# Kernel optimization log

Measured on AMD Instinct MI355X. Metric: run time of the kernel, lower is better.

The kernel has to match this reference:

```python
import jax, jax.numpy as jnp
import numpy as np

NUM_HEADS = 16
THETA = 10000.0


def _rope(x, cos, sin):
    # x: [B, H, S, d_k]; cos/sin: [S, d_k//2]
    x_even = x[..., 0::2]
    x_odd = x[..., 1::2]
    out_even = x_even * cos - x_odd * sin
    out_odd = x_odd * cos + x_even * sin
    # interleave back to original even/odd layout
    return jnp.stack([out_even, out_odd], axis=-1).reshape(x.shape)


def setup_inputs() -> dict:
    key = jax.random.key(0)
    ks = jax.random.split(key, 5)
    B, S, D = 2, 2048, 1024
    std = 2.0 / (D + D)
    return {
        "x": jax.random.normal(ks[0], (B, S, D), dtype=jnp.float32),
        "w_q": jax.random.normal(ks[1], (D, D), dtype=jnp.float32) * std,
        "w_k": jax.random.normal(ks[2], (D, D), dtype=jnp.float32) * std,
        "w_v": jax.random.normal(ks[3], (D, D), dtype=jnp.float32) * std,
        "w_o": jax.random.normal(ks[4], (D, D), dtype=jnp.float32) * std,
    }


def reference(x, w_q, w_k, w_v, w_o):
    B, S, D = x.shape
    H = NUM_HEADS
    d_k = D // H

    # QKV projections: x @ W.T
    q = jnp.einsum('bsd,ed->bse', x, w_q).reshape(B, S, H, d_k).transpose(0, 2, 1, 3)
    k = jnp.einsum('bsd,ed->bse', x, w_k).reshape(B, S, H, d_k).transpose(0, 2, 1, 3)
    v = jnp.einsum('bsd,ed->bse', x, w_v).reshape(B, S, H, d_k).transpose(0, 2, 1, 3)

    # RoPE (token_positions = arange(S))
    pos = jnp.arange(S, dtype=jnp.float32)
    inv_freq = 1.0 / (THETA ** (2.0 * jnp.arange(d_k // 2, dtype=jnp.float32) / d_k))
    angles = pos[:, None] * inv_freq[None, :]  # [S, d_k//2]
    cos, sin = jnp.cos(angles), jnp.sin(angles)
    q = _rope(q, cos, sin)
    k = _rope(k, cos, sin)

    # causal attention
    scores = jnp.einsum('bhqd,bhkd->bhqk', q, k) / jnp.sqrt(jnp.float32(d_k))
    causal = jnp.tril(jnp.ones((S, S), dtype=bool))
    scores = jnp.where(causal[None, None], scores, -jnp.inf)
    attn = jax.nn.softmax(scores, axis=-1)
    out = jnp.einsum('bhqk,bhkd->bhqd', attn, v)  # [B, H, S, d_k]

    out = out.transpose(0, 2, 1, 3).reshape(B, S, D)
    return jnp.einsum('bsd,ed->bse', out, w_o)
```

## Files before the change

### kernel.cpp

```cpp
#include <hip/hip_runtime.h>

typedef unsigned short u16;
typedef unsigned int u32;
typedef short bf16x8 __attribute__((ext_vector_type(8)));
typedef float f32x4 __attribute__((ext_vector_type(4)));

#define CSC 0.18033688011112042f

__device__ __forceinline__ u16 f2bf(float f) {
    union { float f; unsigned u; } x; x.f = f;
    unsigned r = x.u + 0x7fffu + ((x.u >> 16) & 1u);
    return (u16)(r >> 16);
}
__device__ __forceinline__ float bf2f(u16 v) {
    union { unsigned u; float f; } x; x.u = ((unsigned)v) << 16;
    return x.f;
}
__device__ __forceinline__ u32 cvt_pk_bf16(float lo, float hi) {
    u32 r;
    asm("v_cvt_pk_bf16_f32 %0, %1, %2" : "=v"(r) : "v"(lo), "v"(hi));
    return r;
}
__device__ __forceinline__ float exp2_fast(float x) {
#if __has_builtin(__builtin_amdgcn_exp2f)
    return __builtin_amdgcn_exp2f(x);
#else
    return exp2f(x);
#endif
}
__device__ __forceinline__ void gl_lds16(const u16* g, u16* l) {
#if __has_builtin(__builtin_amdgcn_global_load_lds)
    __builtin_amdgcn_global_load_lds(
        (const __attribute__((address_space(1))) unsigned int*)g,
        (__attribute__((address_space(3))) unsigned int*)l, 16, 0, 0);
#else
    *(bf16x8*)l = *(const bf16x8*)g;
#endif
}
__device__ __forceinline__ int ileave(int x) {
    return (x < 16) ? (x << 1) : (((x - 16) << 1) | 1);
}

__global__ void cvt_all_kernel(const float* __restrict__ x, const float* __restrict__ wq,
                               const float* __restrict__ wk, const float* __restrict__ wv,
                               const float* __restrict__ wo,
                               u16* __restrict__ xb, u16* __restrict__ qkvw,
                               u16* __restrict__ ow) {
    int i = blockIdx.x * 256 + threadIdx.x;
    const float4* src;
    ushort4* dst;
    if (i < 1048576) {
        src = (const float4*)x + i;
        dst = (ushort4*)xb + i;
    } else {
        int r = i - 1048576;
        int m = r >> 18;
        int off = r & 262143;
        const float* s4 = (m == 0) ? wq : (m == 1) ? wk : (m == 2) ? wv : wo;
        u16* d = (m < 3) ? (qkvw + (size_t)m * 1048576) : ow;
        src = (const float4*)s4 + off;
        dst = (ushort4*)d + off;
    }
    float4 v = *src;
    ushort4 o;
    o.x = f2bf(v.x); o.y = f2bf(v.y); o.z = f2bf(v.z); o.w = f2bf(v.w);
    *dst = o;
}

__global__ void rope_kernel(u16* __restrict__ qb, u16* __restrict__ kb) {
    int idx = blockIdx.x * 256 + threadIdx.x;
    u16* buf;
    float scale;
    if (blockIdx.y == 0) { buf = qb; scale = CSC; } else { buf = kb; scale = 1.0f; }
    int g   = idx & 7;
    int row = idx >> 3;
    int s   = row & 2047;
    u16* p = buf + (size_t)row * 64 + g * 8;
    bf16x8 v = *(bf16x8*)p;
    bf16x8 o;
    #pragma unroll
    for (int q = 0; q < 4; ++q) {
        int i = g * 4 + q;
        float inv = exp2_fast((float)i * -0.4152410118609203f);
        float ang = (float)s * inv;
        float sn, cs;
        sincosf(ang, &sn, &cs);
        float e  = bf2f(((u16*)&v)[2 * q]);
        float od = bf2f(((u16*)&v)[2 * q + 1]);
        ((u16*)&o)[2 * q]     = f2bf((e * cs - od * sn) * scale);
        ((u16*)&o)[2 * q + 1] = f2bf((od * cs + e * sn) * scale);
    }
    *(bf16x8*)p = o;
}

__global__ __launch_bounds__(256) void gemm_qkv(const u16* __restrict__ A,
                                                const u16* __restrict__ Bw,
                                                u16* __restrict__ C, int K) {
    __shared__ __align__(16) u16 SH[8448];
    u16* As = SH;
    u16* Bs = SH + 4096;
    const int tid  = threadIdx.x;
    const int bm   = blockIdx.x * 128;
    const int bn   = blockIdx.y * 128;
    const int wave = tid >> 6, lane = tid & 63;
    const int wm   = (wave >> 1) * 64, wn = (wave & 1) * 64;
    const int l16  = lane & 15, quad = lane >> 4;
    const int mat  = bn >> 10;

    f32x4 acc[4][4];
    #pragma unroll
    for (int i = 0; i < 4; i++)
        #pragma unroll
        for (int j = 0; j < 4; j++)
            #pragma unroll
            for (int e = 0; e < 4; e++) acc[i][j][e] = 0.0f;

    const int srow = tid >> 2, scol = (tid & 3) * 8;
    const u16* gA0 = A  + (size_t)(bm + srow) * K + scol;
    const u16* gA1 = A  + (size_t)(bm + 64 + srow) * K + scol;
    const u16* gB0 = Bw + (size_t)(bn + srow) * K + scol;
    const u16* gB1 = Bw + (size_t)(bn + 64 + srow) * K + scol;
    u16* lA0 = &As[(size_t)tid * 8];
    u16* lA1 = &As[(size_t)(tid + 256) * 8];
    u16* lB0 = &Bs[(size_t)tid * 8];
    u16* lB1 = &Bs[(size_t)(tid + 256) * 8];

    for (int k0 = 0; k0 < K; k0 += 32) {
        __syncthreads();
        gl_lds16(gA0 + k0, lA0);
        gl_lds16(gA1 + k0, lA1);
        gl_lds16(gB0 + k0, lB0);
        gl_lds16(gB1 + k0, lB1);
        __syncthreads();
        bf16x8 af[4], bfr[4];
        #pragma unroll
        for (int i = 0; i < 4; i++) af[i]  = *(const bf16x8*)&As[(wm + i * 16 + l16) * 32 + quad * 8];
        #pragma unroll
        for (int j = 0; j < 4; j++) bfr[j] = *(const bf16x8*)&Bs[(wn + j * 16 + l16) * 32 + quad * 8];
        #pragma unroll
        for (int i = 0; i < 4; i++)
            #pragma unroll
            for (int j = 0; j < 4; j++)
                acc[i][j] = __builtin_amdgcn_mfma_f32_16x16x32_bf16(af[i], bfr[j], acc[i][j], 0, 0, 0);
    }

    const int b  = bm >> 11, sb = bm & 2047;
    if (mat < 2) {
        #pragma unroll
        for (int pass = 0; pass < 2; ++pass) {
            __syncthreads();
            if ((wn >> 6) == pass) {
                #pragma unroll
                for (int i = 0; i < 4; i++)
                    #pragma unroll
                    for (int j = 0; j < 4; j++)
                        #pragma unroll
                        for (int r = 0; r < 4; r++) {
                            int rl = wm + i * 16 + quad * 4 + r;
                            int cl = j * 16 + l16;
                            SH[rl * 66 + cl] = f2bf(acc[i][j][r]);
                        }
            }
            __syncthreads();
            int rl   = tid >> 1;
            int half = (tid & 1) * 32;
            int c    = (bn + pass * 64) & 1023;
            int h    = c >> 6;
            int s    = sb + rl;
            u16* dst = C + (size_t)mat * 4194304 +
                       (((size_t)(b * 16 + h) * 2048 + s) * 64) + half;
            const u16* srcp = &SH[rl * 66 + half];
            #pragma unroll
            for (int kk = 0; kk < 4; ++kk)
                *(bf16x8*)(dst + kk * 8) = *(const bf16x8*)(srcp + kk * 8);
        }
    } else {
        #pragma unroll
        for (int pass = 0; pass < 2; ++pass) {
            __syncthreads();
            if ((wn >> 6) == pass) {
                #pragma unroll
                for (int i = 0; i < 4; i++)
                    #pragma unroll
                    for (int j = 0; j < 4; j++)
                        #pragma unroll
                        for (int r = 0; r < 4; r++) {
                            int row = j * 16 + l16;
                            int ml  = wm + i * 16 + quad * 4 + r;
                            int sp  = (ml & ~31) | ileave(ml & 31);
                            SH[row * 130 + sp] = f2bf(acc[i][j][r]);
                        }
            }
            __syncthreads();
            int row = tid >> 2, seg = tid & 3;
            int cc  = (bn + pass * 64 + row) & 1023;
            int h = cc >> 6, dv = cc & 63;
            u16* dst = C + (size_t)8388608 +
                       (((size_t)(b * 16 + h) * 64 + dv) * 2048) + sb + seg * 32;
            const u16* srcp = &SH[row * 130 + seg * 32];
            #pragma unroll
            for (int kk = 0; kk < 4; ++kk)
                *(bf16x8*)(dst + kk * 8) = *(const bf16x8*)(srcp + kk * 8);
        }
    }
}

__global__ __launch_bounds__(256, 2) void gemm_out(const u16* __restrict__ A,
                                                   const u16* __restrict__ Bw,
                                                   float* __restrict__ C, int K) {
    __shared__ __align__(16) u16 As[128 * 32];
    __shared__ __align__(16) u16 Bs[64 * 32];
    const int tid  = threadIdx.x;
    const int bm   = blockIdx.x * 128;
    const int bn   = blockIdx.y * 64;
    const int wave = tid >> 6, lane = tid & 63;
    const int wm   = wave * 32;
    const int l16  = lane & 15, quad = lane >> 4;

    f32x4 acc[2][4];
    #pragma unroll
    for (int i = 0; i < 2; i++)
        #pragma unroll
        for (int j = 0; j < 4; j++)
            #pragma unroll
            for (int e = 0; e < 4; e++) acc[i][j][e] = 0.0f;

    const int srow = tid >> 2, scol = (tid & 3) * 8;
    const u16* gA0 = A  + (size_t)(bm + srow) * K + scol;
    const u16* gA1 = A  + (size_t)(bm + 64 + srow) * K + scol;
    const u16* gB0 = Bw + (size_t)(bn + srow) * K + scol;
    u16* lA0 = &As[(size_t)tid * 8];
    u16* lA1 = &As[(size_t)(tid + 256) * 8];
    u16* lB0 = &Bs[(size_t)tid * 8];

    for (int k0 = 0; k0 < K; k0 += 32) {
        __syncthreads();
        gl_lds16(gA0 + k0, lA0);
        gl_lds16(gA1 + k0, lA1);
        gl_lds16(gB0 + k0, lB0);
        __syncthreads();
        bf16x8 af[2], bfr[4];
        #pragma unroll
        for (int i = 0; i < 2; i++) af[i]  = *(const bf16x8*)&As[(wm + i * 16 + l16) * 32 + quad * 8];
        #pragma unroll
        for (int j = 0; j < 4; j++) bfr[j] = *(const bf16x8*)&Bs[(j * 16 + l16) * 32 + quad * 8];
        #pragma unroll
        for (int i = 0; i < 2; i++)
            #pragma unroll
            for (int j = 0; j < 4; j++)
                acc[i][j] = __builtin_amdgcn_mfma_f32_16x16x32_bf16(af[i], bfr[j], acc[i][j], 0, 0, 0);
    }

    #pragma unroll
    for (int i = 0; i < 2; i++)
        #pragma unroll
        for (int j = 0; j < 4; j++)
            #pragma unroll
            for (int r = 0; r < 4; r++) {
                int mr = bm + wm + i * 16 + quad * 4 + r;
                int nc = bn + j * 16 + l16;
                C[(size_t)mr * 1024 + nc] = acc[i][j][r];
            }
}

__global__ __launch_bounds__(256, 2) void attn_kernel(const u16* __restrict__ Q,
                                                      const u16* __restrict__ Kb,
                                                      const u16* __restrict__ Vt,
                                                      u16* __restrict__ Oout) {
    __shared__ __align__(16) u16 KV[2][8192];
    __shared__ __align__(16) u16 PW[8 * 1024];
    const int tid  = threadIdx.x;
    const int wave = tid >> 6, lane = tid & 63;
    const int l16  = lane & 15, quad = lane >> 4;
    const int bid  = blockIdx.x;
    const int j    = (bid >> 3) & 15;
    const int bh   = (bid & 7) * 4 + (bid >> 7);
    const int T    = 32 - j;
    const int qA0  = j * 64 + wave * 16;
    const int qB0  = (31 - j) * 64 + wave * 16;

    const u16* Qh = Q  + (size_t)bh * 2048 * 64;
    const u16* Kh = Kb + (size_t)bh * 2048 * 64;
    const u16* Vh = Vt + (size_t)bh * 64 * 2048;

    bf16x8 qAf0 = *(const bf16x8*)&Qh[(size_t)(qA0 + l16) * 64 + quad * 8];
    bf16x8 qAf1 = *(const bf16x8*)&Qh[(size_t)(qA0 + l16) * 64 + 32 + quad * 8];
    bf16x8 qBf0 = *(const bf16x8*)&Qh[(size_t)(qB0 + l16) * 64 + quad * 8];
    bf16x8 qBf1 = *(const bf16x8*)&Qh[(size_t)(qB0 + l16) * 64 + 32 + quad * 8];

    f32x4 oA[4], oB[4];
    float lsA[4], lsB[4];
    #pragma unroll
    for (int t = 0; t < 4; t++)
        #pragma unroll
        for (int e = 0; e < 4; e++) { oA[t][e] = 0.0f; oB[t][e] = 0.0f; }
    #pragma unroll
    for (int r = 0; r < 4; r++) { lsA[r] = 0.0f; lsB[r] = 0.0f; }

    const int srow = tid >> 2;
    const int scs  = (((tid & 3) ^ ((tid >> 3) & 3))) * 8;
    const u16* gK = Kh + (size_t)srow * 64 + scs;
    const u16* gV = Vh + (size_t)srow * 2048 + scs;

    const int cswz = (quad ^ ((l16 >> 1) & 3)) * 8;
    const int psw0 = ((quad ^ (l16 & 7)) << 3);
    const int psw1 = (((quad ^ (l16 & 7)) ^ 4) << 3);

    u16* pw16B = PW + wave * 2048;
    u16* pw16A = pw16B + 1024;
    u32* pw32B = (u32*)pw16B;
    u32* pw32A = (u32*)pw16A;

    auto stage = [&](int t, int buf) {
        u16* base = KV[buf];
        gl_lds16(gK + (size_t)t * 4096,      base + (size_t)tid * 8);
        gl_lds16(gK + (size_t)t * 4096 + 32, base + 2048 + (size_t)tid * 8);
        gl_lds16(gV + (size_t)t * 64,        base + 4096 + (size_t)tid * 8);
        gl_lds16(gV + (size_t)t * 64 + 32,   base + 6144 + (size_t)tid * 8);
    };

    auto qk_pack = [&](const bf16x8& q0f, const bf16x8& q1f, bf16x8* kf0, bf16x8* kf1,
                       float* ls, u32* pw32, int q0, int kbase, bool diag) {
        f32x4 s[4];
        #pragma unroll
        for (int n = 0; n < 4; n++) {
            #pragma unroll
            for (int e = 0; e < 4; e++) s[n][e] = 0.0f;
            s[n] = __builtin_amdgcn_mfma_f32_16x16x32_bf16(q0f, kf0[n], s[n], 0, 0, 0);
            s[n] = __builtin_amdgcn_mfma_f32_16x16x32_bf16(q1f, kf1[n], s[n], 0, 0, 0);
        }
        float p[4][4];
        #pragma unroll
        for (int n = 0; n < 4; n++)
            #pragma unroll
            for (int r = 0; r < 4; r++) {
                float v = exp2_fast(s[n][r]);
                if (diag) {
                    int row = q0 + quad * 4 + r;
                    v = (kbase + n * 16 + l16 > row) ? 0.0f : v;
                }
                p[n][r] = v;
                ls[r] += v;
            }
        #pragma unroll
        for (int c = 0; c < 2; c++)
            #pragma unroll
            for (int r = 0; r < 4; r++) {
                int prow = quad * 4 + r;
                int pj   = (((c * 4 + (l16 >> 2)) ^ (prow & 7)) << 2) | (l16 & 3);
                pw32[prow * 32 + pj] = cvt_pk_bf16(p[2 * c][r], p[2 * c + 1][r]);
            }
    };

    auto pv = [&](u16* pw16, bf16x8* vf0, bf16x8* vf1, f32x4* o) {
        bf16x8 pf0 = *(const bf16x8*)&pw16[l16 * 64 + psw0];
        bf16x8 pf1 = *(const bf16x8*)&pw16[l16 * 64 + psw1];
        #pragma unroll
        for (int dn = 0; dn < 4; dn++) {
            o[dn] = __builtin_amdgcn_mfma_f32_16x16x32_bf16(pf0, vf0[dn], o[dn], 0, 0, 0);
            o[dn] = __builtin_amdgcn_mfma_f32_16x16x32_bf16(pf1, vf1[dn], o[dn], 0, 0, 0);
        }
    };

    stage(0, 0);
    for (int t = 0; t < T; ++t) {
        __syncthreads();
        if (t + 1 < T) stage(t + 1, (t + 1) & 1);
        const u16* B = KV[t & 1];
        bf16x8 kf0[4], kf1[4], vf0[4], vf1[4];
        #pragma unroll
        for (int n = 0; n < 4; n++) {
            int ri = (n * 16 + l16) * 32 + cswz;
            kf0[n] = *(const bf16x8*)&B[ri];
            kf1[n] = *(const bf16x8*)&B[2048 + ri];
            vf0[n] = *(const bf16x8*)&B[4096 + ri];
            vf1[n] = *(const bf16x8*)&B[6144 + ri];
        }
        const int kbase = t * 64;
        const bool hasA = (t <= j);

        qk_pack(qBf0, qBf1, kf0, kf1, lsB, pw32B, qB0, kbase, t == T - 1);
        if (hasA)
            qk_pack(qAf0, qAf1, kf0, kf1, lsA, pw32A, qA0, kbase, t == j);

        asm volatile("s_waitcnt lgkmcnt(0)" ::: "memory");

        pv(pw16B, vf0, vf1, oB);
        if (hasA)
            pv(pw16A, vf0, vf1, oA);
    }

    #pragma unroll
    for (int off = 1; off < 16; off <<= 1)
        #pragma unroll
        for (int r = 0; r < 4; r++) {
            lsA[r] += __shfl_xor(lsA[r], off);
            lsB[r] += __shfl_xor(lsB[r], off);
        }

    const int b = bh >> 4, h = bh & 15;
    #pragma unroll
    for (int r = 0; r < 4; r++) {
        float iA = 1.0f / lsA[r];
        float iB = 1.0f / lsB[r];
        int sA = qA0 + quad * 4 + r;
        int sB = qB0 + quad * 4 + r;
        #pragma unroll
        for (int dn = 0; dn < 4; dn++) {
            int d = h * 64 + dn * 16 + l16;
            Oout[((size_t)b * 2048 + sA) * 1024 + d] = f2bf(oA[dn][r] * iA);
            Oout[((size_t)b * 2048 + sB) * 1024 + d] = f2bf(oB[dn][r] * iB);
        }
    }
}

extern "C" void kernel_launch(void* const* d_in, const int* in_sizes, int n_in,
                              void* d_out, int out_size, void* d_ws, size_t ws_size,
                              hipStream_t stream) {
    const float* x  = (const float*)d_in[0];
    const float* wq = (const float*)d_in[1];
    const float* wk = (const float*)d_in[2];
    const float* wv = (const float*)d_in[3];
    const float* wo = (const float*)d_in[4];
    float* out = (float*)d_out;

    const int M = 4096, D = 1024;
    u16* xb    = (u16*)d_ws;
    u16* qkvw  = xb   + (size_t)M * D;
    u16* ow    = qkvw + (size_t)3 * D * D;
    u16* qkv   = ow   + (size_t)D * D;
    u16* qb    = qkv;
    u16* kb    = qkv + (size_t)M * D;
    u16* vtb   = qkv + (size_t)2 * M * D;
    u16* aob   = qkv + (size_t)3 * M * D;

    cvt_all_kernel<<<8192, 256, 0, stream>>>(x, wq, wk, wv, wo, xb, qkvw, ow);

    dim3 gq(32, 24);
    gemm_qkv<<<gq, 256, 0, stream>>>(xb, qkvw, qkv, D);

    dim3 gr(2048, 2);
    rope_kernel<<<gr, 256, 0, stream>>>(qb, kb);

    attn_kernel<<<512, 256, 0, stream>>>(qb, kb, vtb, aob);

    dim3 go(32, 16);
    gemm_out<<<go, 256, 0, stream>>>(aob, ow, out, D);
}
```

Measured before the change: 192.9 us.

## Double-buffer LDS tiles and XOR-swizzle columns in projection GEMMs

Both the QKV and output projection GEMMs now ping-pong between two LDS buffers. The next K-slice's global-to-LDS load is issued before the MFMA work on the current slice, which lets the loads overlap compute and removes one barrier per iteration. The 8-element column chunk is also XOR-swizzled by row bits on both the store and the fragment-read sides, to cut LDS bank conflicts on the 32-wide rows. The cost is double the LDS per block, which could lower occupancy, especially for gemm_out with its two-blocks-per-CU launch bound.

```diff
diff --git a/kernel.cpp b/kernel.cpp
--- a/kernel.cpp
+++ b/kernel.cpp
@@ -96,9 +96,8 @@
 __global__ __launch_bounds__(256) void gemm_qkv(const u16* __restrict__ A,
                                                 const u16* __restrict__ Bw,
                                                 u16* __restrict__ C, int K) {
-    __shared__ __align__(16) u16 SH[8448];
-    u16* As = SH;
-    u16* Bs = SH + 4096;
+    __shared__ __align__(16) u16 SB[16384];
+    u16* SH = SB;
     const int tid  = threadIdx.x;
     const int bm   = blockIdx.x * 128;
     const int bn   = blockIdx.y * 128;
@@ -115,33 +114,41 @@
             #pragma unroll
             for (int e = 0; e < 4; e++) acc[i][j][e] = 0.0f;
 
-    const int srow = tid >> 2, scol = (tid & 3) * 8;
+    const int srow = tid >> 2;
+    const int scol = (((tid & 3) ^ ((tid >> 3) & 3))) * 8;
     const u16* gA0 = A  + (size_t)(bm + srow) * K + scol;
     const u16* gA1 = A  + (size_t)(bm + 64 + srow) * K + scol;
     const u16* gB0 = Bw + (size_t)(bn + srow) * K + scol;
     const u16* gB1 = Bw + (size_t)(bn + 64 + srow) * K + scol;
-    u16* lA0 = &As[(size_t)tid * 8];
-    u16* lA1 = &As[(size_t)(tid + 256) * 8];
-    u16* lB0 = &Bs[(size_t)tid * 8];
-    u16* lB1 = &Bs[(size_t)(tid + 256) * 8];
-
+    const int csw = (quad ^ ((l16 >> 1) & 3)) * 8;
+
+    auto stage = [&](int k0, int buf) {
+        u16* As = SB + buf * 8192;
+        u16* Bs = As + 4096;
+        gl_lds16(gA0 + k0, As + (size_t)tid * 8);
+        gl_lds16(gA1 + k0, As + (size_t)(tid + 256) * 8);
+        gl_lds16(gB0 + k0, Bs + (size_t)tid * 8);
+        gl_lds16(gB1 + k0, Bs + (size_t)(tid + 256) * 8);
+    };
+
+    stage(0, 0);
+    int cur = 0;
     for (int k0 = 0; k0 < K; k0 += 32) {
         __syncthreads();
-        gl_lds16(gA0 + k0, lA0);
-        gl_lds16(gA1 + k0, lA1);
-        gl_lds16(gB0 + k0, lB0);
-        gl_lds16(gB1 + k0, lB1);
-        __syncthreads();
+        if (k0 + 32 < K) stage(k0 + 32, cur ^ 1);
+        const u16* As = SB + cur * 8192;
+        const u16* Bs = As + 4096;
         bf16x8 af[4], bfr[4];
         #pragma unroll
-        for (int i = 0; i < 4; i++) af[i]  = *(const bf16x8*)&As[(wm + i * 16 + l16) * 32 + quad * 8];
-        #pragma unroll
-        for (int j = 0; j < 4; j++) bfr[j] = *(const bf16x8*)&Bs[(wn + j * 16 + l16) * 32 + quad * 8];
+        for (int i = 0; i < 4; i++) af[i]  = *(const bf16x8*)&As[(wm + i * 16 + l16) * 32 + csw];
+        #pragma unroll
+        for (int j = 0; j < 4; j++) bfr[j] = *(const bf16x8*)&Bs[(wn + j * 16 + l16) * 32 + csw];
         #pragma unroll
         for (int i = 0; i < 4; i++)
             #pragma unroll
             for (int j = 0; j < 4; j++)
                 acc[i][j] = __builtin_amdgcn_mfma_f32_16x16x32_bf16(af[i], bfr[j], acc[i][j], 0, 0, 0);
+        cur ^= 1;
     }
 
     const int b  = bm >> 11, sb = bm & 2047;
@@ -208,8 +215,7 @@
 __global__ __launch_bounds__(256, 2) void gemm_out(const u16* __restrict__ A,
                                                    const u16* __restrict__ Bw,
                                                    float* __restrict__ C, int K) {
-    __shared__ __align__(16) u16 As[128 * 32];
-    __shared__ __align__(16) u16 Bs[64 * 32];
+    __shared__ __align__(16) u16 SB[12288];
     const int tid  = threadIdx.x;
     const int bm   = blockIdx.x * 128;
     const int bn   = blockIdx.y * 64;
@@ -225,30 +231,38 @@
             #pragma unroll
             for (int e = 0; e < 4; e++) acc[i][j][e] = 0.0f;
 
-    const int srow = tid >> 2, scol = (tid & 3) * 8;
+    const int srow = tid >> 2;
+    const int scol = (((tid & 3) ^ ((tid >> 3) & 3))) * 8;
     const u16* gA0 = A  + (size_t)(bm + srow) * K + scol;
     const u16* gA1 = A  + (size_t)(bm + 64 + srow) * K + scol;
     const u16* gB0 = Bw + (size_t)(bn + srow) * K + scol;
-    u16* lA0 = &As[(size_t)tid * 8];
-    u16* lA1 = &As[(size_t)(tid + 256) * 8];
-    u16* lB0 = &Bs[(size_t)tid * 8];
-
+    const int csw = (quad ^ ((l16 >> 1) & 3)) * 8;
+
+    auto stage = [&](int k0, int buf) {
+        u16* base = SB + buf * 6144;
+        gl_lds16(gA0 + k0, base + (size_t)tid * 8);
+        gl_lds16(gA1 + k0, base + (size_t)(tid + 256) * 8);
+        gl_lds16(gB0 + k0, base + 4096 + (size_t)tid * 8);
+    };
+
+    stage(0, 0);
+    int cur = 0;
     for (int k0 = 0; k0 < K; k0 += 32) {
         __syncthreads();
-        gl_lds16(gA0 + k0, lA0);
-        gl_lds16(gA1 + k0, lA1);
-        gl_lds16(gB0 + k0, lB0);
-        __syncthreads();
+        if (k0 + 32 < K) stage(k0 + 32, cur ^ 1);
+        const u16* As = SB + cur * 6144;
+        const u16* Bs = As + 4096;
         bf16x8 af[2], bfr[4];
         #pragma unroll
-        for (int i = 0; i < 2; i++) af[i]  = *(const bf16x8*)&As[(wm + i * 16 + l16) * 32 + quad * 8];
-        #pragma unroll
-        for (int j = 0; j < 4; j++) bfr[j] = *(const bf16x8*)&Bs[(j * 16 + l16) * 32 + quad * 8];
+        for (int i = 0; i < 2; i++) af[i]  = *(const bf16x8*)&As[(wm + i * 16 + l16) * 32 + csw];
+        #pragma unroll
+        for (int j = 0; j < 4; j++) bfr[j] = *(const bf16x8*)&Bs[(j * 16 + l16) * 32 + csw];
         #pragma unroll
         for (int i = 0; i < 2; i++)
             #pragma unroll
             for (int j = 0; j < 4; j++)
                 acc[i][j] = __builtin_amdgcn_mfma_f32_16x16x32_bf16(af[i], bfr[j], acc[i][j], 0, 0, 0);
+        cur ^= 1;
     }
 
     #pragma unroll
```

Result: faster. 183.6 us (-4.8%).
